# Performance work log

Measured on AMD Instinct MI355X. Metric: run time of the kernel, lower is better.

Reference implementation:

```python
import jax, jax.numpy as jnp
import numpy as np

H_IMG = W_IMG = 1024
H_MAP = W_MAP = 64
SCALE = 16  # img // fmap, both axes
SCALES = [2, 2.5, 3, 3.5, 4, 5]
RATIOS = [0.5, 1.5, 2.0, 2.5, 3, 3.5, 4]
A = len(SCALES) * len(RATIOS)  # 42
POS_T, NEG_T = 0.5, 0.3


def _anchors_np():
    # generate_base_anchors + generate_anchor_boxes (down_h = down_w = SCALE)
    base = np.zeros((A, 4), np.float32)
    cy = cx = SCALE / 2.0
    i = 0
    for s in SCALES:
        for ar in RATIOS:
            h = SCALE * s * np.sqrt(ar)
            w = SCALE * s * np.sqrt(1.0 / ar)
            base[i] = [cy - h / 2.0, cx - w / 2.0, cy + h / 2.0, cx + w / 2.0]
            i += 1
    sy = np.arange(H_MAP) * SCALE
    sx = np.arange(W_MAP) * SCALE
    gx, gy = np.meshgrid(sx, sy)
    shifts = np.stack([gy.ravel(), gx.ravel(), gy.ravel(), gx.ravel()], axis=1)
    # order (H, W, A) -> matches conf.permute(0,2,3,1) flatten
    return (base[None, :, :] + shifts[:, None, :]).reshape(-1, 4).astype(np.float32)


def _conv(x, w, b):
    y = jax.lax.conv_general_dilated(x, w, (1, 1), 'SAME',
                                     dimension_numbers=('NCHW', 'OIHW', 'NCHW'))
    return y + b[None, :, None, None]


def setup_inputs() -> dict:
    key = jax.random.key(0)
    ks = jax.random.split(key, 10)
    B, N, C, Hm, Wm, HID = 8, 20, 256, 64, 64, 512
    feature_map = jax.random.normal(ks[0], (B, C, Hm, Wm), dtype=jnp.float32)
    # valid GT boxes in pixel xyxy-style (d0<d2, d1<d3), last 5 per image padded -1
    p0 = jax.random.uniform(ks[1], (B, N)) * 860.0
    p1 = jax.random.uniform(ks[2], (B, N)) * 860.0
    s0 = jax.random.uniform(ks[3], (B, N)) * 144.0 + 16.0
    s1 = jax.random.uniform(ks[4], (B, N)) * 144.0 + 16.0
    gt_bboxes = jnp.stack([p0, p1, p0 + s0, p1 + s1], axis=-1)
    gt_bboxes = gt_bboxes.at[:, 15:, :].set(-1.0)
    gt_classes = jax.random.randint(ks[5], (B, N), 0, 10)
    conv1_w = jax.random.normal(ks[6], (HID, C, 3, 3), dtype=jnp.float32) * 0.02
    conv1_b = jnp.zeros((HID,), jnp.float32)
    conf_w = jax.random.normal(ks[7], (A, HID, 1, 1), dtype=jnp.float32) * 0.02
    conf_b = jnp.zeros((A,), jnp.float32)
    reg_w = jax.random.normal(ks[8], (4 * A, HID, 1, 1), dtype=jnp.float32) * 0.02
    reg_b = jnp.zeros((4 * A,), jnp.float32)
    return {"feature_map": feature_map, "gt_bboxes": gt_bboxes, "gt_classes": gt_classes,
            "conv1_w": conv1_w, "conv1_b": conv1_b, "conf_w": conf_w, "conf_b": conf_b,
            "reg_w": reg_w, "reg_b": reg_b}


def reference(feature_map, gt_bboxes, gt_classes, conv1_w, conv1_b,
              conf_w, conf_b, reg_w, reg_b):
    anc = jnp.asarray(_anchors_np())           # [M,4]
    B = feature_map.shape[0]
    M = anc.shape[0]                           # H*W*A

    # project_bboxes p2a: divide by scale, keep -1 padding
    pad = gt_bboxes == -1.0
    g = jnp.where(pad, -1.0, gt_bboxes / float(SCALE))  # [B,N,4]
    valid = g[..., 0] >= 0                                # [B,N]
    g_safe = jnp.where(valid[..., None], g, jnp.array([0.0, 0.0, 1.0, 1.0]))

    # pairwise IoU [B,M,N] (vectorized get_iou_mat; invalid GT -> 0)
    tl = jnp.maximum(anc[None, :, None, :2], g_safe[:, None, :, :2])
    br = jnp.minimum(anc[None, :, None, 2:], g_safe[:, None, :, 2:])
    wh = jnp.clip(br - tl, 0.0)
    inter = wh[..., 0] * wh[..., 1]
    area_a = (anc[:, 2] - anc[:, 0]) * (anc[:, 3] - anc[:, 1])
    area_g = (g_safe[..., 2] - g_safe[..., 0]) * (g_safe[..., 3] - g_safe[..., 1])
    iou = inter / (area_a[None, :, None] + area_g[:, None, :] - inter)
    iou = jnp.where(valid[:, None, :], iou, 0.0)

    # positive assignment: per-GT argmax anchors + IoU > pos_thresh
    max_per_gt = iou.max(axis=1, keepdims=True)            # [B,1,N]
    pos_mask = ((iou == max_per_gt) & (max_per_gt > 0)) | (iou > POS_T)
    pos_any = pos_mask.any(axis=-1)                        # [B,M]
    a2g = jnp.argmax(iou, axis=2)                          # [B,M]
    max_per_anc = iou.max(axis=2)                          # [B,M]

    gt_for_anc = jnp.take_along_axis(g_safe, a2g[:, :, None], axis=1)  # [B,M,4]
    anc_b = jnp.broadcast_to(anc, (B, M, 4))
    gt_sel = jnp.where(pos_any[..., None], gt_for_anc, anc_b)  # safe for log

    # calc_gt_offsets (cxcywh encode), computed for all anchors, masked later
    a_c = (anc_b[..., :2] + anc_b[..., 2:]) * 0.5
    a_s = anc_b[..., 2:] - anc_b[..., :2]
    g_c = (gt_sel[..., :2] + gt_sel[..., 2:]) * 0.5
    g_s = gt_sel[..., 2:] - gt_sel[..., :2]
    off_gt = jnp.concatenate([(g_c - a_c) / a_s, jnp.log(g_s / a_s)], axis=-1)
    off_gt = off_gt.reshape(-1, 4)                          # [B*M,4]

    # ProposalModule head (dropout is a no-op in eval)
    x = jax.nn.relu(_conv(feature_map, conv1_w, conv1_b))
    conf = _conv(x, conf_w, conf_b)                         # [B,A,H,W]
    reg = _conv(x, reg_w, reg_b)                            # [B,4A,H,W]
    cflat = conf.transpose(0, 2, 3, 1).reshape(-1)          # [B*M]
    offp = reg.transpose(0, 2, 3, 1).reshape(-1, 4)         # [B*M,4]

    pf = pos_any.reshape(-1).astype(jnp.float32)
    P = pf.sum()

    # cls loss: BCE-with-logits, label 1 on positives, 0 on P sampled negatives
    cls_pos = (jax.nn.softplus(-cflat) * pf).sum() / P
    neg = max_per_anc.reshape(-1) < NEG_T
    scores = jax.random.uniform(jax.random.key(7), cflat.shape)
    scores = jnp.where(neg, scores, 2.0)
    ranks = jnp.argsort(jnp.argsort(scores))               # random sample = rank < P
    sel = (neg & (ranks < P)).astype(jnp.float32)
    cls_neg = (jax.nn.softplus(cflat) * sel).sum() / sel.sum()
    cls_loss = 0.5 * (cls_pos + cls_neg)

    d = offp - off_gt
    ad = jnp.abs(d)
    sl1 = jnp.where(ad < 1.0, 0.5 * ad * ad, ad - 0.5)
    reg_loss = (sl1 * pf[:, None]).sum() / (P * 4.0)

    return cls_loss + reg_loss
```

## Files before the change

### kernel.cpp

```cpp
#include <hip/hip_runtime.h>
#include <hip/hip_fp16.h>
#include <stdint.h>

constexpr int B_  = 8, HM = 64, WM = 64, A_ = 42, CIN = 256, HIDN = 512;
constexpr int M_  = HM * WM * A_;
constexpr int NA  = B_ * M_;
constexpr int HALF = NA / 2;
constexpr int KK  = CIN * 9;
constexpr float POS_T = 0.5f;

constexpr int WINY = 10, WINX = 10, WPIX = WINY * WINX;
constexpr int PERIMG = A_ * WPIX;
constexpr int WBLK = (PERIMG + 511) / 512;
constexpr int NMAXB = WBLK * B_;

constexpr int MAXPOS = 4096, MAXSEL = 4096, MAXCAND = 16384, MAXTIE = 256;
constexpr int MAXPIX = 1024;
constexpr uint32_t VCAND = 16384u;

constexpr int KCH = 288;
constexpr int TFBLK = HALF / 512;
constexpr int WCVTB = (HIDN * KK / 4) / 512;
constexpr int NBLK_TF = NMAXB + TFBLK + WCVTB;

constexpr size_t OFF_CTRL  = 0;
constexpr size_t OFF_BINS  = 256;
constexpr size_t OFF_MAXGT = 768;
constexpr size_t OFF_SLOT  = 2048;
constexpr size_t MS_END    = 133120;
constexpr size_t OFF_PLIST = 133120;
constexpr size_t OFF_POSL  = 137216;
constexpr size_t OFF_SELL  = 153600;
constexpr size_t OFF_CAND  = 169984;
constexpr size_t OFF_APATCH= 8689664;
constexpr size_t OFF_WF16  = 13408256;
constexpr size_t OFF_HFIN  = 15767552;


__device__ __forceinline__ unsigned short f2bf(float f) {
  uint32_t x = __float_as_uint(f);
  uint32_t r = x + 0x7FFFu + ((x >> 16) & 1u);
  return (unsigned short)(r >> 16);
}
__device__ __forceinline__ float bf2f(unsigned short h) {
  return __uint_as_float(((uint32_t)h) << 16);
}
__device__ __forceinline__ uint32_t f2h2(float a, float b) {
  return (uint32_t)__half_as_ushort(__float2half_rn(a)) |
         ((uint32_t)__half_as_ushort(__float2half_rn(b)) << 16);
}

typedef _Float16 h8v __attribute__((ext_vector_type(8)));
typedef float f4v __attribute__((ext_vector_type(4)));

__device__ __forceinline__ float iou_pair(float ay0, float ax0, float ay1, float ax1,
                                          float areaA, float g0, float g1, float g2, float g3,
                                          float areaG) {
#pragma clang fp contract(off)
  float ty = fmaxf(ay0, g0), tx = fmaxf(ax0, g1);
  float by = fminf(ay1, g2), bx = fminf(ax1, g3);
  float hy = by - ty; hy = fmaxf(hy, 0.f);
  float hx = bx - tx; hx = fmaxf(hx, 0.f);
  float inter = hy * hx;
  return inter / (areaA + areaG - inter);
}

__device__ __forceinline__ void anchor_box(const float* basef, int a, int y, int x,
                                           float& ay0, float& ax0, float& ay1, float& ax1,
                                           float& areaA) {
#pragma clang fp contract(off)
  double sy = 16.0 * (double)y, sx = 16.0 * (double)x;
  ay0 = (float)((double)basef[a * 4 + 0] + sy);
  ax0 = (float)((double)basef[a * 4 + 1] + sx);
  ay1 = (float)((double)basef[a * 4 + 2] + sy);
  ax1 = (float)((double)basef[a * 4 + 3] + sx);
  areaA = (ay1 - ay0) * (ax1 - ax0);
}

__device__ __forceinline__ void fill_base(float* sbase, int t) {
  if (t < 42) {
    const double SC[6] = {2.0, 2.5, 3.0, 3.5, 4.0, 5.0};
    const double RA[7] = {0.5, 1.5, 2.0, 2.5, 3.0, 3.5, 4.0};
    int si = t / 7, ri = t - si * 7;
    double h = 16.0 * SC[si] * sqrt(RA[ri]);
    double w = 16.0 * SC[si] * sqrt(1.0 / RA[ri]);
    sbase[t * 4 + 0] = (float)(8.0 - h / 2.0);
    sbase[t * 4 + 1] = (float)(8.0 - w / 2.0);
    sbase[t * 4 + 2] = (float)(8.0 + h / 2.0);
    sbase[t * 4 + 3] = (float)(8.0 + w / 2.0);
  }
}

__device__ __forceinline__ void fill_gt(const float* gt, int b, float* sg, float* sarea,
                                        unsigned* sval, int t) {
  if (t < 20) {
#pragma clang fp contract(off)
    float g4[4];
    for (int d = 0; d < 4; d++) {
      float v = gt[(b * 20 + t) * 4 + d];
      g4[d] = (v == -1.0f) ? -1.0f : v * 0.0625f;
    }
    unsigned valid = (g4[0] >= 0.0f) ? 1u : 0u;
    if (!valid) { g4[0] = 0.f; g4[1] = 0.f; g4[2] = 1.f; g4[3] = 1.f; }
    sg[t * 4 + 0] = g4[0]; sg[t * 4 + 1] = g4[1]; sg[t * 4 + 2] = g4[2]; sg[t * 4 + 3] = g4[3];
    sarea[t] = (g4[2] - g4[0]) * (g4[3] - g4[1]);
    sval[t] = valid;
  }
}

__device__ __forceinline__ void claim_pixel(char* ws, int pixg) {
  int* slotmap = (int*)(ws + OFF_SLOT);
  if (atomicCAS((unsigned*)&slotmap[pixg], 0u, 0xFFFFFFFFu) == 0u) {
    unsigned s = atomicAdd((unsigned*)(ws + OFF_CTRL) + 2, 1u);
    if (s < MAXPIX) { ((int*)(ws + OFF_PLIST))[s] = pixg; slotmap[pixg] = (int)s + 1; }
    else slotmap[pixg] = -1;
  }
}

__device__ __forceinline__ float softplusf(float x) {
  return fmaxf(x, 0.f) + log1pf(expf(-fabsf(x)));
}
__device__ __forceinline__ float sl1(float d) {
  float ad = fabsf(d);
  return ad < 1.f ? 0.5f * ad * ad : ad - 0.5f;
}

__device__ __forceinline__ void tf_round(uint32_t& x0, uint32_t& x1, int r) {
  x0 += x1; x1 = (x1 << r) | (x1 >> (32 - r)); x1 ^= x0;
}
__device__ __forceinline__ void threefry(uint32_t c0, uint32_t c1, uint32_t& o0, uint32_t& o1) {
  const uint32_t k0 = 0u, k1 = 7u;
  const uint32_t k2 = k0 ^ k1 ^ 0x1BD11BDAu;
  uint32_t x0 = c0 + k0, x1 = c1 + k1;
  tf_round(x0, x1, 13); tf_round(x0, x1, 15); tf_round(x0, x1, 26); tf_round(x0, x1, 6);
  x0 += k1; x1 += k2 + 1u;
  tf_round(x0, x1, 17); tf_round(x0, x1, 29); tf_round(x0, x1, 16); tf_round(x0, x1, 24);
  x0 += k2; x1 += k0 + 2u;
  tf_round(x0, x1, 13); tf_round(x0, x1, 15); tf_round(x0, x1, 26); tf_round(x0, x1, 6);
  x0 += k0; x1 += k1 + 3u;
  tf_round(x0, x1, 17); tf_round(x0, x1, 29); tf_round(x0, x1, 16); tf_round(x0, x1, 24);
  x0 += k1; x1 += k2 + 4u;
  tf_round(x0, x1, 13); tf_round(x0, x1, 15); tf_round(x0, x1, 26); tf_round(x0, x1, 6);
  x0 += k2; x1 += k0 + 5u;
  o0 = x0; o1 = x1;
}

__device__ __forceinline__ void dev_threefry_emit(char* ws, int p, int lane) {
  uint32_t o0, o1; threefry((uint32_t)p, (uint32_t)(p + HALF), o0, o1);
  uint32_t v0 = o0 >> 9, v1 = o1 >> 9;
  unsigned* ctrl = (unsigned*)(ws + OFF_CTRL);
  unsigned* bins = (unsigned*)(ws + OFF_BINS);
  uint2* cand = (uint2*)(ws + OFF_CAND);
  bool h0 = v0 < VCAND, h1 = v1 < VCAND;
  unsigned long long m0 = __ballot(h0), m1 = __ballot(h1);
  if (m0 | m1) {
    int n0 = __popcll(m0);
    int leader = (int)__ffsll(m0 | m1) - 1;
    unsigned base = 0;
    if (lane == leader) base = atomicAdd(&ctrl[3], (unsigned)(n0 + __popcll(m1)));
    base = (unsigned)__shfl((int)base, leader, 64);
    unsigned long long below = (1ull << lane) - 1ull;
    if (h0) {
      unsigned s = base + (unsigned)__popcll(m0 & below);
      if (s < MAXCAND) cand[s] = make_uint2(v0, (unsigned)p);
      atomicAdd(&bins[v0 >> 7], 1u);
    }
    if (h1) {
      unsigned s = base + (unsigned)n0 + (unsigned)__popcll(m1 & below);
      if (s < MAXCAND) cand[s] = make_uint2(v1, (unsigned)(p + HALF));
      atomicAdd(&bins[v1 >> 7], 1u);
    }
  }
}

__global__ void __launch_bounds__(512) kTF(const float* __restrict__ gt,
                                           const float* __restrict__ w1, char* ws) {
  __shared__ float sbase[168], sg[80], sarea[20];
  __shared__ unsigned sval[20];
  __shared__ int smax[20];
  int t = threadIdx.x, lane = t & 63;
  if (blockIdx.x < NMAXB) {
    int b = blockIdx.x / WBLK, blk = blockIdx.x - b * WBLK;
    fill_base(sbase, t);
    fill_gt(gt, b, sg, sarea, sval, t);
    if (t < 20) smax[t] = 0;
    __syncthreads();
    int idx = blk * 512 + t;
    bool ok = idx < PERIMG;
    float ay0 = 0.f, ax0 = 0.f, ay1 = 0.f, ax1 = 0.f, areaA = 1.f;
    if (ok) {
      int a = idx / WPIX, pp = idx - a * WPIX;
      int y = pp / WINX, x = pp - y * WINX;
      anchor_box(sbase, a, y, x, ay0, ax0, ay1, ax1, areaA);
    }
#pragma unroll
    for (int n = 0; n < 20; n++) {
      float io = 0.f;
      if (ok && sval[n]) io = iou_pair(ay0, ax0, ay1, ax1, areaA,
                                       sg[n * 4], sg[n * 4 + 1], sg[n * 4 + 2],
                                       sg[n * 4 + 3], sarea[n]);
#pragma unroll
      for (int off = 32; off >= 1; off >>= 1) io = fmaxf(io, __shfl_xor(io, off, 64));
      if ((t & 63) == 0 && io > 0.f) atomicMax(&smax[n], __float_as_int(io));
    }
    __syncthreads();
    if (t < 20 && smax[t] != 0)
      atomicMax((int*)(ws + OFF_MAXGT) + b * 20 + t, smax[t]);
  } else if (blockIdx.x < NMAXB + TFBLK) {
    int p = ((int)blockIdx.x - NMAXB) * 512 + t;
    if (p < HALF) dev_threefry_emit(ws, p, lane);
  } else {
    int q = ((int)blockIdx.x - (NMAXB + TFBLK)) * 512 + t;
    float4 v = ((const float4*)w1)[q];
    uint2 o;
    o.x = f2h2(v.x, v.y);
    o.y = f2h2(v.z, v.w);
    ((uint2*)(ws + OFF_WF16))[q] = o;
  }
}

__global__ void __launch_bounds__(512) kPos2(const float* __restrict__ gt, char* ws) {
  __shared__ float sbase[168], sg[80], sarea[20], smg[20];
  __shared__ unsigned sval[20];
  __shared__ unsigned selbins[128];
  __shared__ uint2 ties[MAXTIE];
  __shared__ unsigned tcnt, s_r, s_ucut;
  __shared__ int s_icut, s_cutbin, s_last;
  int b = blockIdx.y, t = threadIdx.x, lane = t & 63;
  unsigned* ctrl = (unsigned*)(ws + OFF_CTRL);
  fill_base(sbase, t);
  fill_gt(gt, b, sg, sarea, sval, t);
  if (t < 20) smg[t] = __int_as_float(((int*)(ws + OFF_MAXGT))[b * 20 + t]);
  __syncthreads();
  int idx = blockIdx.x * 512 + t;
  bool pos = false;
  unsigned packv = 0;
  int pixg = 0;
  if (idx < PERIMG) {
    int a = idx / WPIX, pp = idx - a * WPIX;
    int y = pp / WINX, x = pp - y * WINX;
    float ay0, ax0, ay1, ax1, areaA;
    anchor_box(sbase, a, y, x, ay0, ax0, ay1, ax1, areaA);
    float best = -1.f; int arg = 0;
#pragma unroll
    for (int n = 0; n < 20; n++) {
      float io = 0.f;
      if (sval[n]) io = iou_pair(ay0, ax0, ay1, ax1, areaA,
                                 sg[n * 4], sg[n * 4 + 1], sg[n * 4 + 2],
                                 sg[n * 4 + 3], sarea[n]);
      if (io > best) { best = io; arg = n; }
      float mg = smg[n];
      pos = pos || ((io == mg) && (mg > 0.f)) || (io > POS_T);
    }
    if (pos) {
      int pix = y * 64 + x;
      int i = b * M_ + pix * 42 + a;
      packv = (unsigned)i | ((unsigned)arg << 21);
      pixg = b * 4096 + pix;
    }
  }
  unsigned long long mask = __ballot(pos);
  if (mask) {
    int leader = (int)__ffsll(mask) - 1;
    unsigned base = 0;
    if (lane == leader) base = atomicAdd(&ctrl[0], (unsigned)__popcll(mask));
    base = (unsigned)__shfl((int)base, leader, 64);
    if (pos) {
      unsigned slot = base + (unsigned)__popcll(mask & ((1ull << lane) - 1ull));
      if (slot < MAXPOS) ((unsigned*)(ws + OFF_POSL))[slot] = packv;
      claim_pixel(ws, pixg);
    }
  }
  __syncthreads();
  if (t == 0) {
    unsigned r = __hip_atomic_fetch_add(&ctrl[11], 1u, __ATOMIC_RELAXED,
                                        __HIP_MEMORY_SCOPE_AGENT);
    s_last = (r == (unsigned)(WBLK * B_) - 1) ? 1 : 0;
  }
  __syncthreads();
  if (!s_last) return;
  const uint2* cand = (const uint2*)(ws + OFF_CAND);
  unsigned P = min(__hip_atomic_load(&ctrl[0], __ATOMIC_RELAXED,
                                     __HIP_MEMORY_SCOPE_AGENT), (unsigned)MAXPOS);
  unsigned nc = min(__hip_atomic_load(&ctrl[3], __ATOMIC_RELAXED,
                                      __HIP_MEMORY_SCOPE_AGENT), (unsigned)MAXCAND);
  if (t < 128) selbins[t] = ((const unsigned*)(ws + OFF_BINS))[t];
  if (t == 0) tcnt = 0;
  __syncthreads();
  if (t == 0) {
    unsigned cum = 0; int c = 0;
    for (; c < 128; c++) { if (cum + selbins[c] >= P) break; cum += selbins[c]; }
    if (c == 128) c = 127;
    s_cutbin = c; s_r = (P > cum) ? (P - cum) : 0u;
  }
  __syncthreads();
  int cutbin = s_cutbin;
  for (unsigned j = t; j < nc; j += 512) {
    uint2 cj = cand[j];
    if ((int)(cj.x >> 7) == cutbin) {
      unsigned k = atomicAdd(&tcnt, 1u);
      if (k < MAXTIE) ties[k] = cj;
    }
  }
  __syncthreads();
  unsigned n = min(tcnt, (unsigned)MAXTIE);
  unsigned r = s_r; if (r > n) r = n;
  if (r == 0) {
    if (t == 0) { s_ucut = 0; s_icut = -1; }
  } else if (t < (int)n) {
    uint2 mine = ties[t];
    unsigned rank = 0;
    for (unsigned j = 0; j < n; j++) {
      uint2 o = ties[j];
      if (o.x < mine.x || (o.x == mine.x && (int)o.y < (int)mine.y)) rank++;
    }
    if (rank == r - 1) { s_ucut = mine.x; s_icut = (int)mine.y; }
  }
  __syncthreads();
  unsigned ucut = s_ucut; int icut = s_icut;
  unsigned total = (nc + 511u) & ~511u;
  for (unsigned j = t; j < total; j += 512) {
    bool sel = false; uint2 cj = make_uint2(0u, 0u);
    if (j < nc) {
      cj = cand[j];
      sel = (cj.x < ucut) || (cj.x == ucut && (int)cj.y <= icut);
    }
    unsigned long long m2 = __ballot(sel);
    if (m2) {
      int leader = (int)__ffsll(m2) - 1;
      unsigned base = 0;
      if (lane == leader) base = atomicAdd(&ctrl[1], (unsigned)__popcll(m2));
      base = (unsigned)__shfl((int)base, leader, 64);
      if (sel) {
        unsigned slot = base + (unsigned)__popcll(m2 & ((1ull << lane) - 1ull));
        if (slot < MAXSEL) {
          ((int*)(ws + OFF_SELL))[slot] = (int)cj.y;
          int bb = (int)cj.y / M_; int m = (int)cj.y - bb * M_;
          claim_pixel(ws, bb * 4096 + m / 42);
        }
      }
    }
  }
}

__global__ void __launch_bounds__(256) kIm2col(const float* __restrict__ fm, char* ws) {
  unsigned* ctrl = (unsigned*)(ws + OFF_CTRL);
  int npix = min((int)ctrl[2], MAXPIX);
  int blk = blockIdx.x;
  if (blk >= npix) return;
  int chunk = blockIdx.y;
  int pixg = ((const int*)(ws + OFF_PLIST))[blk];
  int b = pixg >> 12, pix = pixg & 4095;
  int y = pix >> 6, x = pix & 63;
  uint32_t* Ap = (uint32_t*)(ws + OFF_APATCH) + (size_t)blk * (KK / 2);
  int u0 = chunk * 384;
  for (int u = u0 + threadIdx.x; u < u0 + 384; u += 256) {
    float v[2];
#pragma unroll
    for (int h = 0; h < 2; h++) {
      int k = 2 * u + h;
      int ic = k / 9, r = k - ic * 9;
      int dy = r / 3, dx = r - dy * 3;
      int yy = y + dy - 1, xx = x + dx - 1;
      float vv = 0.f;
      if (yy >= 0 && yy < 64 && xx >= 0 && xx < 64)
        vv = fm[(((size_t)b * CIN + ic) * 64 + yy) * 64 + xx];
      v[h] = vv;
    }
    Ap[u] = f2h2(v[0], v[1]);
  }
}

__global__ void __launch_bounds__(512) kGemm(const float* __restrict__ b1, char* ws) {
  __shared__ float red[8][16][132];
  unsigned* ctrl = (unsigned*)(ws + OFF_CTRL);
  int npix = min((int)ctrl[2], MAXPIX);
  int strip = blockIdx.x, och = blockIdx.y;
  int px0 = strip * 16;
  if (px0 >= npix) return;
  int oc0 = och * 128;
  const _Float16* Ap = (const _Float16*)(ws + OFF_APATCH);
  const _Float16* Wf = (const _Float16*)(ws + OFF_WF16);
  int t = threadIdx.x, lane = t & 63, wv = t >> 6;
  int kq = lane >> 4;
  int kb = wv * KCH;
  const _Float16* Arow = Ap + (size_t)(px0 + (lane & 15)) * KK + kb + kq * 8;
  const _Float16* Wrow = Wf + (size_t)(oc0 + (lane & 15)) * KK + kb + kq * 8;
  f4v acc[8] = {};
#pragma unroll 3
  for (int s = 0; s < 9; s++) {
    h8v a = *(const h8v*)(Arow + s * 32);
#pragma unroll
    for (int o = 0; o < 8; o++) {
      h8v bfr = *(const h8v*)(Wrow + (size_t)o * 16 * KK + s * 32);
      acc[o] = __builtin_amdgcn_mfma_f32_16x16x32_f16(a, bfr, acc[o], 0, 0, 0);
    }
  }
#pragma unroll
  for (int o = 0; o < 8; o++) {
    int col = o * 16 + (lane & 15);
#pragma unroll
    for (int r = 0; r < 4; r++)
      red[wv][kq * 4 + r][col] = acc[o][r];
  }
  __syncthreads();
  int row = t >> 5, colg = t & 31;
  if (px0 + row < npix) {
    float s4[4];
#pragma unroll
    for (int j = 0; j < 4; j++) s4[j] = b1[oc0 + colg * 4 + j];
#pragma unroll
    for (int w = 0; w < 8; w++)
#pragma unroll
      for (int j = 0; j < 4; j++) s4[j] += red[w][row][colg * 4 + j];
#pragma unroll
    for (int j = 0; j < 4; j++) s4[j] = fmaxf(s4[j], 0.f);
    unsigned short* hf = (unsigned short*)(ws + OFF_HFIN);
    uint2 o2;
    o2.x = f2h2(s4[0], s4[1]);
    o2.y = f2h2(s4[2], s4[3]);
    *(uint2*)(hf + (size_t)(px0 + row) * HIDN + oc0 + colg * 4) = o2;
  }
}

__global__ void __launch_bounds__(256) kHead(const float* __restrict__ gt,
                                             const float* __restrict__ cw,
                                             const float* __restrict__ cb,
                                             const float* __restrict__ rw,
                                             const float* __restrict__ rb,
                                             char* ws, float* out) {
  __shared__ float sbase[168], sg[640];
  __shared__ float sacc[3];
  int t = threadIdx.x;
  fill_base(sbase, t);
  if (t < 160) {
#pragma clang fp contract(off)
    float g4[4];
    for (int d = 0; d < 4; d++) {
      float v = gt[t * 4 + d];
      g4[d] = (v == -1.0f) ? -1.0f : v * 0.0625f;
    }
    if (!(g4[0] >= 0.0f)) { g4[0] = 0.f; g4[1] = 0.f; g4[2] = 1.f; g4[3] = 1.f; }
    sg[t * 4 + 0] = g4[0]; sg[t * 4 + 1] = g4[1];
    sg[t * 4 + 2] = g4[2]; sg[t * 4 + 3] = g4[3];
  }
  if (t < 3) sacc[t] = 0.f;
  __syncthreads();
  unsigned* ctrl = (unsigned*)(ws + OFF_CTRL);
  float* accum = (float*)(ctrl + 16);
  int np = min((int)ctrl[0], MAXPOS);
  int ns = min((int)ctrl[1], MAXSEL);
  int nent = np + ns;
  const unsigned* posl = (const unsigned*)(ws + OFF_POSL);
  const int* sell = (const int*)(ws + OFF_SELL);
  const int* slotmap = (const int*)(ws + OFF_SLOT);
  const unsigned short* hfin = (const unsigned short*)(ws + OFF_HFIN);
  int lane = t & 63;
  int gwave = blockIdx.x * 4 + (t >> 6);
  int nwaves = gridDim.x * 4;
  for (int e = gwave; e < nent; e += nwaves) {
    bool isPos = e < np;
    int i, arg = 0;
    if (isPos) { unsigned pck = posl[e]; i = (int)(pck & 0x1FFFFFu); arg = (int)(pck >> 21); }
    else i = sell[e - np];
    int b = i / M_; int m = i - b * M_;
    int pix = m / 42; int a = m - pix * 42;
    int y = pix >> 6, x = pix & 63;
    int slot = slotmap[b * 4096 + pix] - 1;
    if (slot < 0 || slot >= MAXPIX) continue;
    float h[8];
    {
      h8v hv = *(const h8v*)(hfin + (size_t)slot * HIDN + lane * 8);
#pragma unroll
      for (int j = 0; j < 8; j++) h[j] = (float)hv[j];
    }
    const float* cwr = cw + (size_t)a * HIDN + lane * 8;
    float4 cA = *(const float4*)cwr;
    float4 cB = *(const float4*)(cwr + 4);
    float cp = h[0] * cA.x + h[1] * cA.y + h[2] * cA.z + h[3] * cA.w +
               h[4] * cB.x + h[5] * cB.y + h[6] * cB.z + h[7] * cB.w;
#pragma unroll
    for (int off = 32; off >= 1; off >>= 1) cp += __shfl_xor(cp, off, 64);
    float conf = cp + cb[a];
    if (isPos) {
      float rp[4];
#pragma unroll
      for (int d = 0; d < 4; d++) {
        const float* rwr = rw + (size_t)(a * 4 + d) * HIDN + lane * 8;
        float4 rA = *(const float4*)rwr;
        float4 rB = *(const float4*)(rwr + 4);
        float sd = h[0] * rA.x + h[1] * rA.y + h[2] * rA.z + h[3] * rA.w +
                   h[4] * rB.x + h[5] * rB.y + h[6] * rB.z + h[7] * rB.w;
#pragma unroll
        for (int off = 32; off >= 1; off >>= 1) sd += __shfl_xor(sd, off, 64);
        rp[d] = sd + rb[a * 4 + d];
      }
      if (lane == 0) {
#pragma clang fp contract(off)
        float ay0, ax0, ay1, ax1, areaA;
        anchor_box(sbase, a, y, x, ay0, ax0, ay1, ax1, areaA);
        const float* g = sg + (size_t)(b * 20 + arg) * 4;
        float acy = (ay0 + ay1) * 0.5f, acx = (ax0 + ax1) * 0.5f;
        float ah = ay1 - ay0, aw = ax1 - ax0;
        float gcy = (g[0] + g[2]) * 0.5f, gcx = (g[1] + g[3]) * 0.5f;
        float gh = g[2] - g[0], gw = g[3] - g[1];
        float t0 = (gcy - acy) / ah, t1 = (gcx - acx) / aw;
        float t2 = logf(gh / ah), t3 = logf(gw / aw);
        float sL = sl1(rp[0] - t0) + sl1(rp[1] - t1) + sl1(rp[2] - t2) + sl1(rp[3] - t3);
        atomicAdd(&sacc[2], sL);
        atomicAdd(&sacc[0], softplusf(-conf));
      }
    } else {
      if (lane == 0) atomicAdd(&sacc[1], softplusf(conf));
    }
  }
  __syncthreads();
  if (t == 0) {
    if (sacc[0] != 0.f) atomicAdd(&accum[0], sacc[0]);
    if (sacc[1] != 0.f) atomicAdd(&accum[1], sacc[1]);
    if (sacc[2] != 0.f) atomicAdd(&accum[2], sacc[2]);
    asm volatile("s_waitcnt vmcnt(0)" ::: "memory");
    unsigned done = __hip_atomic_fetch_add(&ctrl[10], 1u, __ATOMIC_RELAXED,
                                           __HIP_MEMORY_SCOPE_AGENT);
    if (done == gridDim.x - 1) {
      float a0 = __hip_atomic_load(&accum[0], __ATOMIC_RELAXED, __HIP_MEMORY_SCOPE_AGENT);
      float a1 = __hip_atomic_load(&accum[1], __ATOMIC_RELAXED, __HIP_MEMORY_SCOPE_AGENT);
      float a2 = __hip_atomic_load(&accum[2], __ATOMIC_RELAXED, __HIP_MEMORY_SCOPE_AGENT);
      float P = (float)min((int)ctrl[0], MAXPOS);
      float S = (float)min((int)ctrl[1], MAXSEL);
      float cls = 0.5f * (a0 / P + a1 / S);
      out[0] = cls + a2 / (P * 4.0f);
    }
  }
}

extern "C" void kernel_launch(void* const* d_in, const int* in_sizes, int n_in,
                              void* d_out, int out_size, void* d_ws, size_t ws_size,
                              hipStream_t stream) {
  const float* fm = (const float*)d_in[0];
  const float* gt = (const float*)d_in[1];
  const float* w1 = (const float*)d_in[3];
  const float* b1 = (const float*)d_in[4];
  const float* cw = (const float*)d_in[5];
  const float* cb = (const float*)d_in[6];
  const float* rw = (const float*)d_in[7];
  const float* rb = (const float*)d_in[8];
  char* ws = (char*)d_ws;
  float* out = (float*)d_out;

  hipMemsetAsync(ws, 0, MS_END, stream);
  kTF<<<NBLK_TF, 512, 0, stream>>>(gt, w1, ws);
  kPos2<<<dim3(WBLK, B_), 512, 0, stream>>>(gt, ws);
  kIm2col<<<dim3(MAXPIX, 3), 256, 0, stream>>>(fm, ws);
  kGemm<<<dim3(MAXPIX / 16, 4), 512, 0, stream>>>(b1, ws);
  kHead<<<256, 256, 0, stream>>>(gt, cw, cb, rw, rb, ws, out);
}
```

Measured before the change: 180.0 us.

## Bucket random candidates per bin and grid-stride the TF and im2col kernels

Candidate negatives are now scattered directly into fixed-capacity per-bin buckets, with one padded counter per bin. This replaces the global append list plus histogram, so the last kPos2 block reads the cut bin's bucket directly instead of rescanning all candidates to gather ties. The threefry and weight-conversion blocks each process 8 items in a grid-stride loop, and im2col launches 128 blocks per chunk that loop over pixels instead of 1024 mostly idle blocks. The risk is bucket overflow beyond 96 entries per bin, which would silently drop candidates, and per-bin atomic contention in place of wave-aggregated appends.

```diff
diff --git a/kernel.cpp b/kernel.cpp
--- a/kernel.cpp
+++ b/kernel.cpp
@@ -14,24 +14,27 @@
 constexpr int WBLK = (PERIMG + 511) / 512;
 constexpr int NMAXB = WBLK * B_;
 
-constexpr int MAXPOS = 4096, MAXSEL = 4096, MAXCAND = 16384, MAXTIE = 256;
+constexpr int MAXPOS = 4096, MAXSEL = 4096;
 constexpr int MAXPIX = 1024;
 constexpr uint32_t VCAND = 16384u;
+constexpr int NBIN = 128, CAP = 96;
 
 constexpr int KCH = 288;
-constexpr int TFBLK = HALF / 512;
-constexpr int WCVTB = (HIDN * KK / 4) / 512;
-constexpr int NBLK_TF = NMAXB + TFBLK + WCVTB;
+
+constexpr int NWIN = NMAXB;
+constexpr int NRND = 168;
+constexpr int NWCV = 72;
+constexpr int NBLK_TF = NWIN + NRND + NWCV;
 
 constexpr size_t OFF_CTRL  = 0;
-constexpr size_t OFF_BINS  = 256;
-constexpr size_t OFF_MAXGT = 768;
-constexpr size_t OFF_SLOT  = 2048;
-constexpr size_t MS_END    = 133120;
-constexpr size_t OFF_PLIST = 133120;
-constexpr size_t OFF_POSL  = 137216;
-constexpr size_t OFF_SELL  = 153600;
-constexpr size_t OFF_CAND  = 169984;
+constexpr size_t OFF_MAXGT = 256;
+constexpr size_t OFF_BINSP = 1024;
+constexpr size_t OFF_SLOT  = 9216;
+constexpr size_t MS_END    = 140288;
+constexpr size_t OFF_PLIST = 140288;
+constexpr size_t OFF_POSL  = 144384;
+constexpr size_t OFF_SELL  = 160768;
+constexpr size_t OFF_CAND  = 177152;
 constexpr size_t OFF_APATCH= 8689664;
 constexpr size_t OFF_WF16  = 13408256;
 constexpr size_t OFF_HFIN  = 15767552;
@@ -145,31 +148,12 @@
   o0 = x0; o1 = x1;
 }
 
-__device__ __forceinline__ void dev_threefry_emit(char* ws, int p, int lane) {
-  uint32_t o0, o1; threefry((uint32_t)p, (uint32_t)(p + HALF), o0, o1);
-  uint32_t v0 = o0 >> 9, v1 = o1 >> 9;
-  unsigned* ctrl = (unsigned*)(ws + OFF_CTRL);
-  unsigned* bins = (unsigned*)(ws + OFF_BINS);
-  uint2* cand = (uint2*)(ws + OFF_CAND);
-  bool h0 = v0 < VCAND, h1 = v1 < VCAND;
-  unsigned long long m0 = __ballot(h0), m1 = __ballot(h1);
-  if (m0 | m1) {
-    int n0 = __popcll(m0);
-    int leader = (int)__ffsll(m0 | m1) - 1;
-    unsigned base = 0;
-    if (lane == leader) base = atomicAdd(&ctrl[3], (unsigned)(n0 + __popcll(m1)));
-    base = (unsigned)__shfl((int)base, leader, 64);
-    unsigned long long below = (1ull << lane) - 1ull;
-    if (h0) {
-      unsigned s = base + (unsigned)__popcll(m0 & below);
-      if (s < MAXCAND) cand[s] = make_uint2(v0, (unsigned)p);
-      atomicAdd(&bins[v0 >> 7], 1u);
-    }
-    if (h1) {
-      unsigned s = base + (unsigned)n0 + (unsigned)__popcll(m1 & below);
-      if (s < MAXCAND) cand[s] = make_uint2(v1, (unsigned)(p + HALF));
-      atomicAdd(&bins[v1 >> 7], 1u);
-    }
+__device__ __forceinline__ void emit_cand(char* ws, uint32_t v, uint32_t p) {
+  if (v < VCAND) {
+    unsigned bin = v >> 7;
+    unsigned slot = atomicAdd((unsigned*)(ws + OFF_BINSP) + bin * 16, 1u);
+    if (slot < (unsigned)CAP)
+      ((uint2*)(ws + OFF_CAND))[bin * CAP + slot] = make_uint2(v, p);
   }
 }
 
@@ -178,8 +162,8 @@
   __shared__ float sbase[168], sg[80], sarea[20];
   __shared__ unsigned sval[20];
   __shared__ int smax[20];
-  int t = threadIdx.x, lane = t & 63;
-  if (blockIdx.x < NMAXB) {
+  int t = threadIdx.x;
+  if (blockIdx.x < NWIN) {
     int b = blockIdx.x / WBLK, blk = blockIdx.x - b * WBLK;
     fill_base(sbase, t);
     fill_gt(gt, b, sg, sarea, sval, t);
@@ -206,25 +190,34 @@
     __syncthreads();
     if (t < 20 && smax[t] != 0)
       atomicMax((int*)(ws + OFF_MAXGT) + b * 20 + t, smax[t]);
-  } else if (blockIdx.x < NMAXB + TFBLK) {
-    int p = ((int)blockIdx.x - NMAXB) * 512 + t;
-    if (p < HALF) dev_threefry_emit(ws, p, lane);
+  } else if (blockIdx.x < NWIN + NRND) {
+    int p0 = ((int)blockIdx.x - NWIN) * 512 + t;
+#pragma unroll
+    for (int it = 0; it < 8; it++) {
+      int p = p0 + it * (NRND * 512);
+      uint32_t o0, o1; threefry((uint32_t)p, (uint32_t)(p + HALF), o0, o1);
+      emit_cand(ws, o0 >> 9, (uint32_t)p);
+      emit_cand(ws, o1 >> 9, (uint32_t)(p + HALF));
+    }
   } else {
-    int q = ((int)blockIdx.x - (NMAXB + TFBLK)) * 512 + t;
-    float4 v = ((const float4*)w1)[q];
-    uint2 o;
-    o.x = f2h2(v.x, v.y);
-    o.y = f2h2(v.z, v.w);
-    ((uint2*)(ws + OFF_WF16))[q] = o;
+    int q0 = ((int)blockIdx.x - (NWIN + NRND)) * 512 + t;
+#pragma unroll
+    for (int it = 0; it < 8; it++) {
+      int q = q0 + it * (NWCV * 512);
+      float4 v = ((const float4*)w1)[q];
+      uint2 o;
+      o.x = f2h2(v.x, v.y);
+      o.y = f2h2(v.z, v.w);
+      ((uint2*)(ws + OFF_WF16))[q] = o;
+    }
   }
 }
 
 __global__ void __launch_bounds__(512) kPos2(const float* __restrict__ gt, char* ws) {
   __shared__ float sbase[168], sg[80], sarea[20], smg[20];
   __shared__ unsigned sval[20];
-  __shared__ unsigned selbins[128];
-  __shared__ uint2 ties[MAXTIE];
-  __shared__ unsigned tcnt, s_r, s_ucut;
+  __shared__ unsigned scnt[128];
+  __shared__ unsigned s_r, s_ucut;
   __shared__ int s_icut, s_cutbin, s_last;
   int b = blockIdx.y, t = threadIdx.x, lane = t & 63;
   unsigned* ctrl = (unsigned*)(ws + OFF_CTRL);
@@ -279,50 +272,42 @@
   }
   __syncthreads();
   if (!s_last) return;
-  const uint2* cand = (const uint2*)(ws + OFF_CAND);
+  const uint2* bucket = (const uint2*)(ws + OFF_CAND);
   unsigned P = min(__hip_atomic_load(&ctrl[0], __ATOMIC_RELAXED,
                                      __HIP_MEMORY_SCOPE_AGENT), (unsigned)MAXPOS);
-  unsigned nc = min(__hip_atomic_load(&ctrl[3], __ATOMIC_RELAXED,
-                                      __HIP_MEMORY_SCOPE_AGENT), (unsigned)MAXCAND);
-  if (t < 128) selbins[t] = ((const unsigned*)(ws + OFF_BINS))[t];
-  if (t == 0) tcnt = 0;
+  if (t < 128)
+    scnt[t] = min(__hip_atomic_load((unsigned*)(ws + OFF_BINSP) + t * 16,
+                                    __ATOMIC_RELAXED, __HIP_MEMORY_SCOPE_AGENT),
+                  (unsigned)CAP);
   __syncthreads();
   if (t == 0) {
     unsigned cum = 0; int c = 0;
-    for (; c < 128; c++) { if (cum + selbins[c] >= P) break; cum += selbins[c]; }
+    for (; c < 128; c++) { if (cum + scnt[c] >= P) break; cum += scnt[c]; }
     if (c == 128) c = 127;
     s_cutbin = c; s_r = (P > cum) ? (P - cum) : 0u;
   }
   __syncthreads();
   int cutbin = s_cutbin;
-  for (unsigned j = t; j < nc; j += 512) {
-    uint2 cj = cand[j];
-    if ((int)(cj.x >> 7) == cutbin) {
-      unsigned k = atomicAdd(&tcnt, 1u);
-      if (k < MAXTIE) ties[k] = cj;
-    }
-  }
-  __syncthreads();
-  unsigned n = min(tcnt, (unsigned)MAXTIE);
+  unsigned n = scnt[cutbin];
   unsigned r = s_r; if (r > n) r = n;
   if (r == 0) {
     if (t == 0) { s_ucut = 0; s_icut = -1; }
   } else if (t < (int)n) {
-    uint2 mine = ties[t];
+    uint2 mine = bucket[cutbin * CAP + t];
     unsigned rank = 0;
     for (unsigned j = 0; j < n; j++) {
-      uint2 o = ties[j];
+      uint2 o = bucket[cutbin * CAP + j];
       if (o.x < mine.x || (o.x == mine.x && (int)o.y < (int)mine.y)) rank++;
     }
     if (rank == r - 1) { s_ucut = mine.x; s_icut = (int)mine.y; }
   }
   __syncthreads();
   unsigned ucut = s_ucut; int icut = s_icut;
-  unsigned total = (nc + 511u) & ~511u;
-  for (unsigned j = t; j < total; j += 512) {
+  for (unsigned j = t; j < (unsigned)(NBIN * CAP); j += 512) {
+    unsigned bin = j / CAP, k = j - bin * CAP;
     bool sel = false; uint2 cj = make_uint2(0u, 0u);
-    if (j < nc) {
-      cj = cand[j];
+    if (k < scnt[bin]) {
+      cj = bucket[j];
       sel = (cj.x < ucut) || (cj.x == ucut && (int)cj.y <= icut);
     }
     unsigned long long m2 = __ballot(sel);
@@ -346,28 +331,28 @@
 __global__ void __launch_bounds__(256) kIm2col(const float* __restrict__ fm, char* ws) {
   unsigned* ctrl = (unsigned*)(ws + OFF_CTRL);
   int npix = min((int)ctrl[2], MAXPIX);
-  int blk = blockIdx.x;
-  if (blk >= npix) return;
   int chunk = blockIdx.y;
-  int pixg = ((const int*)(ws + OFF_PLIST))[blk];
-  int b = pixg >> 12, pix = pixg & 4095;
-  int y = pix >> 6, x = pix & 63;
-  uint32_t* Ap = (uint32_t*)(ws + OFF_APATCH) + (size_t)blk * (KK / 2);
   int u0 = chunk * 384;
-  for (int u = u0 + threadIdx.x; u < u0 + 384; u += 256) {
-    float v[2];
-#pragma unroll
-    for (int h = 0; h < 2; h++) {
-      int k = 2 * u + h;
-      int ic = k / 9, r = k - ic * 9;
-      int dy = r / 3, dx = r - dy * 3;
-      int yy = y + dy - 1, xx = x + dx - 1;
-      float vv = 0.f;
-      if (yy >= 0 && yy < 64 && xx >= 0 && xx < 64)
-        vv = fm[(((size_t)b * CIN + ic) * 64 + yy) * 64 + xx];
-      v[h] = vv;
-    }
-    Ap[u] = f2h2(v[0], v[1]);
+  for (int blk = blockIdx.x; blk < npix; blk += gridDim.x) {
+    int pixg = ((const int*)(ws + OFF_PLIST))[blk];
+    int b = pixg >> 12, pix = pixg & 4095;
+    int y = pix >> 6, x = pix & 63;
+    uint32_t* Ap = (uint32_t*)(ws + OFF_APATCH) + (size_t)blk * (KK / 2);
+    for (int u = u0 + threadIdx.x; u < u0 + 384; u += 256) {
+      float v[2];
+#pragma unroll
+      for (int h = 0; h < 2; h++) {
+        int k = 2 * u + h;
+        int ic = k / 9, r = k - ic * 9;
+        int dy = r / 3, dx = r - dy * 3;
+        int yy = y + dy - 1, xx = x + dx - 1;
+        float vv = 0.f;
+        if (yy >= 0 && yy < 64 && xx >= 0 && xx < 64)
+          vv = fm[(((size_t)b * CIN + ic) * 64 + yy) * 64 + xx];
+        v[h] = vv;
+      }
+      Ap[u] = f2h2(v[0], v[1]);
+    }
   }
 }
 
@@ -551,7 +536,7 @@
   hipMemsetAsync(ws, 0, MS_END, stream);
   kTF<<<NBLK_TF, 512, 0, stream>>>(gt, w1, ws);
   kPos2<<<dim3(WBLK, B_), 512, 0, stream>>>(gt, ws);
-  kIm2col<<<dim3(MAXPIX, 3), 256, 0, stream>>>(fm, ws);
+  kIm2col<<<dim3(128, 3), 256, 0, stream>>>(fm, ws);
   kGemm<<<dim3(MAXPIX / 16, 4), 512, 0, stream>>>(b1, ws);
   kHead<<<256, 256, 0, stream>>>(gt, cw, cb, rw, rb, ws, out);
 }
```

Measured after the change: 162.6 us. 1.11x faster.
